# Kernel optimization log

Hardware: AMD Instinct MI355X
Metric: run time of the kernel (lower is better)

## Reference

```python
import jax, jax.numpy as jnp
from jax import lax
import numpy as np

K_TOP = 100
NMS_THRESH = 0.5
SUBJECT_CATEGORY_ID = 0


def box_cxcywh_to_xyxy(b):
    cx, cy, w, h = b[..., 0], b[..., 1], b[..., 2], b[..., 3]
    return jnp.stack([cx - 0.5 * w, cy - 0.5 * h, cx + 0.5 * w, cy + 0.5 * h], axis=-1)


def _pairwise_iou(boxes):
    # boxes: [K,4] xyxy; uses the +1 pixel convention from the original numpy NMS
    x1, y1, x2, y2 = boxes[:, 0], boxes[:, 1], boxes[:, 2], boxes[:, 3]
    area = (x2 - x1 + 1.0) * (y2 - y1 + 1.0)
    xx1 = jnp.maximum(x1[:, None], x1[None, :])
    yy1 = jnp.maximum(y1[:, None], y1[None, :])
    xx2 = jnp.minimum(x2[:, None], x2[None, :])
    yy2 = jnp.minimum(y2[:, None], y2[None, :])
    w = jnp.maximum(0.0, xx2 - xx1 + 1.0)
    h = jnp.maximum(0.0, yy2 - yy1 + 1.0)
    inter = w * h
    union = area[:, None] + area[None, :] - inter
    return inter / union


def _nms_keep(sub_boxes, obj_boxes, obj_labels, hoi_scores):
    # Greedy grouped pairwise NMS for one image.
    # Grouping key degenerates to object label (subject cat and verb-row are constant).
    K = sub_boxes.shape[0]
    max_scores = hoi_scores.max(axis=-1)
    order = jnp.argsort(-max_scores)
    ovr = _pairwise_iou(sub_boxes) * _pairwise_iou(obj_boxes)  # [K,K]
    same_group = obj_labels[:, None] == obj_labels[None, :]
    ovr = jnp.where(same_group, ovr, 0.0)
    ovr_s = ovr[order][:, order]
    upper = jnp.triu(jnp.ones((K, K), dtype=bool), k=1)
    sup_mat = (ovr_s > NMS_THRESH) & upper  # suppression only of later (lower-score) items

    def body(i, st):
        suppressed, keep = st
        ki = jnp.logical_not(suppressed[i])
        keep = keep.at[i].set(ki)
        suppressed = suppressed | (ki & sup_mat[i])
        return suppressed, keep

    _, keep_sorted = lax.fori_loop(0, K, body, (jnp.zeros(K, bool), jnp.zeros(K, bool)))
    return jnp.zeros(K, bool).at[order].set(keep_sorted)


def setup_inputs() -> dict:
    key = jax.random.key(0)
    k1, k2, k3, k4, k5, k6 = jax.random.split(key, 6)
    B, Q, C, V = 256, 300, 81, 117
    return {
        "pred_obj_logits": jax.random.normal(k1, (B, Q, C), dtype=jnp.float32),
        "pred_verb_logits": jax.random.normal(k2, (B, Q, V), dtype=jnp.float32),
        "pred_sub_boxes": jax.random.uniform(k3, (B, Q, 4), dtype=jnp.float32),
        "pred_obj_boxes": jax.random.uniform(k4, (B, Q, 4), dtype=jnp.float32),
        "correct_mat": (jax.random.uniform(k5, (V, C), dtype=jnp.float32) > 0.3).astype(jnp.float32),
        "target_sizes": jax.random.randint(k6, (B, 2), 200, 640, dtype=jnp.int32),
    }


def reference(pred_obj_logits, pred_verb_logits, pred_sub_boxes, pred_obj_boxes, correct_mat, target_sizes):
    B, Q, C = pred_obj_logits.shape
    V = pred_verb_logits.shape[-1]

    obj_prob = jax.nn.softmax(pred_obj_logits, axis=-1)       # [B,Q,C]  (no_obj=False)
    verb_scores = jax.nn.sigmoid(pred_verb_logits)            # [B,Q,V]

    topk_values, topk_indexes = lax.top_k(obj_prob.reshape(B, Q * C), K_TOP)  # [B,100]
    topk_boxes = topk_indexes // C
    obj_labels = topk_indexes % C

    vs = jnp.take_along_axis(verb_scores, topk_boxes[..., None], axis=1)      # [B,100,V]
    ob = jnp.take_along_axis(pred_obj_boxes, topk_boxes[..., None], axis=1)   # [B,100,4]
    sb = jnp.take_along_axis(pred_sub_boxes, topk_boxes[..., None], axis=1)

    img_h = target_sizes[:, 0].astype(jnp.float32)
    img_w = target_sizes[:, 1].astype(jnp.float32)
    scale_fct = jnp.stack([img_w, img_h, img_w, img_h], axis=1)  # [B,4]
    sub_boxes = box_cxcywh_to_xyxy(sb) * scale_fct[:, None, :]
    obj_boxes = box_cxcywh_to_xyxy(ob) * scale_fct[:, None, :]

    hoi_scores = vs * topk_values[..., None]                    # [B,100,V]
    # masks[b,k,v] = correct_mat[v, obj_labels[b,k]]
    masks = correct_mat.T[obj_labels]                           # [B,100,V]
    hoi_scores = hoi_scores * masks

    keep = jax.vmap(_nms_keep)(sub_boxes, obj_boxes, obj_labels, hoi_scores)  # [B,100] bool
    final_scores = hoi_scores * keep[..., None].astype(hoi_scores.dtype)

    return final_scores, topk_values, obj_labels, sub_boxes, obj_boxes, keep
```

## Files before the change

### kernel.cpp

```cpp
#include <hip/hip_runtime.h>
#include <cmath>

#pragma clang fp contract(off)

#define NT 1024
constexpr int B_ = 256, Q_ = 300, C_ = 81, V_ = 117, K_ = 100;
constexpr int QC_ = Q_ * C_;
constexpr int KV_ = K_ * V_;
constexpr int CAP = 1024;
constexpr int CMN = V_ * C_;

using u32 = unsigned int;
using u64 = unsigned long long;
using u16 = unsigned short;
using u8  = unsigned char;

constexpr u32 PCUT_BITS = 0x3C000000u;
constexpr int BIN0 = 480;
constexpr int NB   = 64;
constexpr int HREP = 8;

constexpr int OFF_CM   = 0;
constexpr int OFF_HIST = 37920;
constexpr int OFF_RMAX = OFF_HIST + 8192;
constexpr int OFF_RINV = OFF_RMAX + 1240;
constexpr int OFF_BSUB = OFF_RINV + 1240;
constexpr int OFF_BOBJ = OFF_BSUB + 1600;
constexpr int OFF_SUPR = OFF_BOBJ + 1600;
constexpr int OFF_SELV = OFF_SUPR + 1600;
constexpr int OFF_SELI = OFF_SELV + 400;
constexpr int OFF_MAXB = OFF_SELI + 400;
constexpr int OFF_ORD  = OFF_MAXB + 400;
constexpr int OFF_LAB  = OFF_ORD + 104;
constexpr int OFF_MISC = OFF_LAB + 104;
constexpr int SMEM_SZ  = OFF_MISC + 48;
static_assert(SMEM_SZ <= 65536, "LDS overflow");
static_assert((OFF_BSUB & 15) == 0 && (OFF_BOBJ & 15) == 0, "b128 align");
static_assert(OFF_HIST >= OFF_CM + CMN * 4, "cm/hist overlap");
static_assert((OFF_HIST & 15) == 0, "cand/hist align");

__device__ __forceinline__ void bar_lds() {
    asm volatile("s_waitcnt lgkmcnt(0)\n\ts_barrier" ::: "memory");
}

__device__ __forceinline__ int RM(int r) { return r + (r >> 5); }

__device__ __forceinline__ u64 shfl_xor_u64(u64 v, int mask) {
    u32 lo = (u32)v, hi = (u32)(v >> 32);
    lo = (u32)__shfl_xor((int)lo, mask, 64);
    hi = (u32)__shfl_xor((int)hi, mask, 64);
    return ((u64)hi << 32) | lo;
}

template <int CTRL>
__device__ __forceinline__ int dpp_i(int x) {
    return __builtin_amdgcn_update_dpp(0, x, CTRL, 0xF, 0xF, true);
}
__device__ __forceinline__ float bfly16(float x){ return __int_as_float(__builtin_amdgcn_ds_swizzle(__float_as_int(x), 0x401F)); }
__device__ __forceinline__ float bfly8 (float x){ return __int_as_float(dpp_i<0x128>(__float_as_int(x))); }
__device__ __forceinline__ float bfly4 (float x){ return __int_as_float(__builtin_amdgcn_ds_swizzle(__float_as_int(x), 0x101F)); }
__device__ __forceinline__ float bfly2 (float x){ return __int_as_float(dpp_i<0x4E>(__float_as_int(x))); }
__device__ __forceinline__ float bfly1 (float x){ return __int_as_float(dpp_i<0xB1>(__float_as_int(x))); }
__device__ __forceinline__ int ibfly4(int x){ return __builtin_amdgcn_ds_swizzle(x, 0x101F); }
__device__ __forceinline__ int ibfly2(int x){ return dpp_i<0x4E>(x); }
__device__ __forceinline__ int ibfly1(int x){ return dpp_i<0xB1>(x); }

__device__ __forceinline__ float iou4(float4 a, float4 b, float areaSum) {
    float xx1 = fmaxf(a.x, b.x);
    float yy1 = fmaxf(a.y, b.y);
    float xx2 = fminf(a.z, b.z);
    float yy2 = fminf(a.w, b.w);
    float w = fmaxf(0.f, xx2 - xx1 + 1.f);
    float h = fmaxf(0.f, yy2 - yy1 + 1.f);
    float inter = w * h;
    return inter / (areaSum - inter);
}

__global__ __launch_bounds__(NT, 4) void hoi_kernel(
    const float* __restrict__ obj_logits,
    const float* __restrict__ verb_logits,
    const float* __restrict__ sub_boxes_in,
    const float* __restrict__ obj_boxes_in,
    const float* __restrict__ cm,
    const int*   __restrict__ tsizes,
    float* __restrict__ out)
{
    const int b = blockIdx.x;
    const int tid = threadIdx.x;

    __shared__ __align__(16) u8 smem[SMEM_SZ];
    float* cml     = (float*)(smem + OFF_CM);
    u32*   hist    = (u32*)(smem + OFF_HIST);
    u64*   cand    = (u64*)(smem + OFF_HIST);
    float* asub    = (float*)(smem + OFF_HIST);
    float* aobj    = (float*)(smem + OFF_HIST + 512);
    float* rowmax  = (float*)(smem + OFF_RMAX);
    float* rinv    = (float*)(smem + OFF_RINV);
    float (*bsub)[4]   = (float(*)[4])(smem + OFF_BSUB);
    float (*bobj)[4]   = (float(*)[4])(smem + OFF_BOBJ);
    u32   (*supcol)[4] = (u32(*)[4])(smem + OFF_SUPR);
    float* sel_val = (float*)(smem + OFF_SELV);
    u32*   sel_idx = (u32*)(smem + OFF_SELI);
    u32*   maxbits = (u32*)(smem + OFF_MAXB);
    u8*    order8  = (u8*)(smem + OFF_ORD);
    u8*    lab8    = (u8*)(smem + OFF_LAB);
    u32*   skeep     = (u32*)(smem + OFF_MISC);
    u32*   keep_bits = (u32*)(smem + OFF_MISC + 16);
    u32*   s_cnt     = (u32*)(smem + OFF_MISC + 32);
    int*   sT        = (int*)(smem + OFF_MISC + 36);
    u64*   wred    = (u64*)(smem + OFF_BOBJ);
    u64*   s_prev  = (u64*)(smem + OFF_SUPR);

    const float* lg = obj_logits + (size_t)b * QC_;

    float* o0 = out;
    float* o1 = out + (size_t)B_ * KV_;
    float* o2 = o1 + (size_t)B_ * K_;
    float* o3 = o2 + (size_t)B_ * K_;
    float* o4 = o3 + (size_t)B_ * K_ * 4;
    float* o5 = o4 + (size_t)B_ * K_ * 4;

    if (tid < NB * HREP) hist[tid] = 0;
    if (tid == 0) *s_cnt = 0;
    bar_lds();

    const int g = tid >> 5, l = tid & 31;
    const bool have2 = (l < C_ - 64);
    const int hsub = tid & (HREP - 1);
    u32 cmask = 0;
    {
        float v0[10], v1[10], v2[10];
        #pragma unroll
        for (int s = 0; s < 10; ++s) {
            int r = g + 32 * s;
            const float* row = lg + (size_t)((r < Q_ ? r : Q_ - 1) * C_);
            v0[s] = row[l];
            v1[s] = row[l + 32];
            v2[s] = have2 ? row[l + 64] : -INFINITY;
        }
        float m[10];
        #pragma unroll
        for (int s = 0; s < 10; ++s) m[s] = fmaxf(fmaxf(v0[s], v1[s]), v2[s]);
        #pragma unroll
        for (int s = 0; s < 10; ++s) m[s] = fmaxf(m[s], bfly16(m[s]));
        #pragma unroll
        for (int s = 0; s < 10; ++s) m[s] = fmaxf(m[s], bfly8(m[s]));
        #pragma unroll
        for (int s = 0; s < 10; ++s) m[s] = fmaxf(m[s], bfly4(m[s]));
        #pragma unroll
        for (int s = 0; s < 10; ++s) m[s] = fmaxf(m[s], bfly2(m[s]));
        #pragma unroll
        for (int s = 0; s < 10; ++s) m[s] = fmaxf(m[s], bfly1(m[s]));
        float e0[10], e1[10], e2[10], sm[10];
        #pragma unroll
        for (int s = 0; s < 10; ++s) {
            e0[s] = expf(v0[s] - m[s]);
            e1[s] = expf(v1[s] - m[s]);
            e2[s] = have2 ? expf(v2[s] - m[s]) : 0.f;
            sm[s] = e0[s] + e1[s] + e2[s];
        }
        #pragma unroll
        for (int s = 0; s < 10; ++s) sm[s] += bfly16(sm[s]);
        #pragma unroll
        for (int s = 0; s < 10; ++s) sm[s] += bfly8(sm[s]);
        #pragma unroll
        for (int s = 0; s < 10; ++s) sm[s] += bfly4(sm[s]);
        #pragma unroll
        for (int s = 0; s < 10; ++s) sm[s] += bfly2(sm[s]);
        #pragma unroll
        for (int s = 0; s < 10; ++s) sm[s] += bfly1(sm[s]);
        #pragma unroll
        for (int s = 0; s < 10; ++s) {
            int r = g + 32 * s;
            if (r < Q_) {
                float ri = 1.f / sm[s];
                float p0 = e0[s] * ri, p1 = e1[s] * ri;
                u32 x0 = __float_as_uint(p0), x1 = __float_as_uint(p1);
                if (x0 >= PCUT_BITS) {
                    atomicAdd(&hist[(((x0 >> 21) - BIN0) << 3) + hsub], 1u);
                    cmask |= 1u << (3 * s);
                }
                if (x1 >= PCUT_BITS) {
                    atomicAdd(&hist[(((x1 >> 21) - BIN0) << 3) + hsub], 1u);
                    cmask |= 1u << (3 * s + 1);
                }
                if (have2) {
                    float p2 = e2[s] * ri;
                    u32 x2 = __float_as_uint(p2);
                    if (x2 >= PCUT_BITS) {
                        atomicAdd(&hist[(((x2 >> 21) - BIN0) << 3) + hsub], 1u);
                        cmask |= 1u << (3 * s + 2);
                    }
                }
                if (l == 0) { rowmax[RM(r)] = m[s]; rinv[RM(r)] = ri; }
            }
        }
    }
    bar_lds();

    if (tid < 64) {
        uint4 ha = ((const uint4*)hist)[tid * 2];
        uint4 hb = ((const uint4*)hist)[tid * 2 + 1];
        u32 suf = ha.x + ha.y + ha.z + ha.w + hb.x + hb.y + hb.z + hb.w;
        #pragma unroll
        for (int off = 1; off < 64; off <<= 1) {
            u32 o = (u32)__shfl_down((int)suf, off, 64);
            suf += (tid + off < 64) ? o : 0;
        }
        u32 nxt = (u32)__shfl_down((int)suf, 1, 64);
        if (tid == 63) nxt = 0;
        if (suf >= (u32)K_ && nxt < (u32)K_) *sT = BIN0 + tid;
    }
    bar_lds();
    const int T = *sT;

    u32 mk = cmask;
    while (mk) {
        int bpos = (int)__builtin_ctz(mk);
        mk &= mk - 1;
        int s = (bpos * 171) >> 9;
        int c = bpos - 3 * s;
        int r = g + 32 * s;
        int col = l + 32 * c;
        int i = r * C_ + col;
        float p = expf(lg[i] - rowmax[RM(r)]) * rinv[RM(r)];
        u32 xb = __float_as_uint(p);
        if ((int)(xb >> 21) >= T) {
            u32 pos = atomicAdd(s_cnt, 1u);
            if (pos < (u32)CAP)
                cand[pos] = ((u64)xb << 32) | (u32)(~i);
        }
    }
    bar_lds();
    const int ncand = (int)*s_cnt;

    constexpr int CM4 = CMN / 4;
    const float4* cmg4 = (const float4*)cm;
    float4 cc0 = cmg4[tid];
    float4 cc1 = cmg4[tid + NT];
    float4 cc2 = (tid < CM4 - 2 * NT) ? cmg4[tid + 2 * NT]
                                      : make_float4(0.f, 0.f, 0.f, 0.f);
    float ctail = (tid == 0) ? cm[CMN - 1] : 0.f;

    if (ncand <= CAP) {
        if (tid < ncand) {
            u64 mykey = cand[tid];
            int rank = 0;
            int f = 0;
            for (; f + 4 <= ncand; f += 4) {
                u64 k0 = cand[f], k1 = cand[f + 1];
                u64 k2 = cand[f + 2], k3 = cand[f + 3];
                rank += (k0 > mykey) ? 1 : 0;
                rank += (k1 > mykey) ? 1 : 0;
                rank += (k2 > mykey) ? 1 : 0;
                rank += (k3 > mykey) ? 1 : 0;
            }
            for (; f < ncand; ++f) rank += (cand[f] > mykey) ? 1 : 0;
            if (rank < K_) {
                sel_val[rank] = __uint_as_float((u32)(mykey >> 32));
                sel_idx[rank] = ~(u32)mykey;
            }
        }
    } else {
        if (tid == 0) *s_prev = ~0ull;
        __syncthreads();
        for (int r = 0; r < K_; r++) {
            u64 prev = *s_prev;
            u64 local = 0;
            for (int i = tid; i < QC_; i += NT) {
                int q = i / C_;
                float p = expf(lg[i] - rowmax[RM(q)]) * rinv[RM(q)];
                u64 key = ((u64)__float_as_uint(p) << 32) | (u32)(~i);
                if (key < prev && key > local) local = key;
            }
            for (int off = 32; off > 0; off >>= 1) {
                u64 o = shfl_xor_u64(local, off);
                if (o > local) local = o;
            }
            if ((tid & 63) == 0) wred[tid >> 6] = local;
            __syncthreads();
            if (tid == 0) {
                u64 m = wred[0];
                for (int wv = 1; wv < 16; wv++) if (wred[wv] > m) m = wred[wv];
                *s_prev = m;
                u32 idx = ~(u32)m;
                if (idx >= (u32)QC_) idx = 0;
                sel_val[r] = __uint_as_float((u32)(m >> 32));
                sel_idx[r] = idx;
            }
            __syncthreads();
        }
    }

    ((float4*)cml)[tid] = cc0;
    ((float4*)cml)[tid + NT] = cc1;
    if (tid < CM4 - 2 * NT) ((float4*)cml)[tid + 2 * NT] = cc2;
    if (tid == 0) cml[CMN - 1] = ctail;
    bar_lds();

    if (tid < 800) {
        int c = tid >> 3, j = tid & 7;
        u32 idx = sel_idx[c];
        int q = (int)idx / C_, lab = (int)idx - q * C_;
        const float* vrow = verb_logits + ((size_t)b * Q_ + q) * V_;
        float* orow = o0 + (size_t)b * KV_ + c * V_;
        float sv = sel_val[c];
        float m = 0.f;
        #pragma unroll
        for (int k = 0; k < 15; ++k) {
            int v = j + 8 * k;
            if (v < V_) {
                float x = vrow[v];
                float cv = cml[v * C_ + lab];
                float hv = (1.f / (1.f + expf(-x))) * sv * cv;
                orow[v] = hv;
                m = fmaxf(m, hv);
            }
        }
        m = fmaxf(m, bfly4(m));
        m = fmaxf(m, bfly2(m));
        m = fmaxf(m, bfly1(m));
        if (j == 0) { maxbits[c] = __float_as_uint(m); lab8[c] = (u8)lab; }
    } else if (tid < 900) {
        int t = tid - 800;
        int idx = (int)sel_idx[t];
        int q = idx / C_;
        float iw = (float)tsizes[b * 2 + 1];
        float ih = (float)tsizes[b * 2 + 0];
        float4 sb = ((const float4*)sub_boxes_in)[(size_t)b * Q_ + q];
        float x1 = (sb.x - 0.5f * sb.z) * iw, y1 = (sb.y - 0.5f * sb.w) * ih;
        float x2 = (sb.x + 0.5f * sb.z) * iw, y2 = (sb.y + 0.5f * sb.w) * ih;
        bsub[t][0] = x1; bsub[t][1] = y1; bsub[t][2] = x2; bsub[t][3] = y2;
        asub[t] = (x2 - x1 + 1.f) * (y2 - y1 + 1.f);
        supcol[t][0] = 0; supcol[t][1] = 0; supcol[t][2] = 0; supcol[t][3] = 0;
    } else if (tid < 1000) {
        int t = tid - 900;
        int idx = (int)sel_idx[t];
        int q = idx / C_;
        float iw = (float)tsizes[b * 2 + 1];
        float ih = (float)tsizes[b * 2 + 0];
        float4 ob = ((const float4*)obj_boxes_in)[(size_t)b * Q_ + q];
        float x1 = (ob.x - 0.5f * ob.z) * iw, y1 = (ob.y - 0.5f * ob.w) * ih;
        float x2 = (ob.x + 0.5f * ob.z) * iw, y2 = (ob.y + 0.5f * ob.w) * ih;
        bobj[t][0] = x1; bobj[t][1] = y1; bobj[t][2] = x2; bobj[t][3] = y2;
        aobj[t] = (x2 - x1 + 1.f) * (y2 - y1 + 1.f);
    } else if (tid < 1004) {
        keep_bits[tid - 1000] = 0;
    }
    bar_lds();

    if (tid < 800) {
        int r = tid >> 3, j = tid & 7;
        u64 kr = ((u64)maxbits[r] << 32) | (u32)(~r);
        int rank = 0;
        for (int k = 0; k < 13; k++) {
            int jj = j * 13 + k;
            if (jj < K_) {
                u64 kj = ((u64)maxbits[jj] << 32) | (u32)(~jj);
                rank += (kj > kr) ? 1 : 0;
            }
        }
        rank += ibfly4(rank);
        rank += ibfly2(rank);
        rank += ibfly1(rank);
        if (j == 0) order8[rank] = (u8)r;
    }
    bar_lds();

    if (tid < K_) {
        o1[(size_t)b * K_ + tid] = sel_val[tid];
        o2[(size_t)b * K_ + tid] = (float)(sel_idx[tid] % (u32)C_);
    }
    if (tid >= 128 && tid < 128 + K_ * 4) {
        int t = tid - 128;
        int r = t >> 2, k = t & 3;
        o3[((size_t)b * K_) * 4 + t] = bsub[r][k];
        o4[((size_t)b * K_) * 4 + t] = bobj[r][k];
    }

    for (int e = tid; e < K_ * K_; e += NT) {
        int i = e / K_, j = e - i * K_;
        if (j > i) {
            int ri = order8[i], rj = order8[j];
            u32 li = lab8[ri], lj = lab8[rj];
            if (li == lj) {
                float4 s_i = *(const float4*)bsub[ri];
                float4 s_j = *(const float4*)bsub[rj];
                float4 b_i = *(const float4*)bobj[ri];
                float4 b_j = *(const float4*)bobj[rj];
                float o = iou4(s_i, s_j, asub[ri] + asub[rj]) *
                          iou4(b_i, b_j, aobj[ri] + aobj[rj]);
                if (o > 0.5f)
                    atomicOr(&supcol[j][i >> 5], 1u << (i & 31));
            }
        }
    }
    bar_lds();

    if (tid < 64) {
        u32 cA[4], cB[4];
        #pragma unroll
        for (int w = 0; w < 4; ++w) cA[w] = supcol[tid][w];
        #pragma unroll
        for (int w = 0; w < 4; ++w) cB[w] = (tid < K_ - 64) ? supcol[tid + 64][w] : 0u;
        bool sA = false, sB = false;
        u32 km[4] = {0, 0, 0, 0};
        #pragma unroll
        for (int i = 0; i < 64; ++i) {
            u64 bal = __ballot(sA);
            if (!((bal >> i) & 1)) {
                km[i >> 5] |= 1u << (i & 31);
                sA = sA || ((cA[i >> 5] >> (i & 31)) & 1u);
                sB = sB || ((cB[i >> 5] >> (i & 31)) & 1u);
            }
        }
        #pragma unroll
        for (int i = 64; i < K_; ++i) {
            u64 bal = __ballot(sB);
            if (!((bal >> (i - 64)) & 1)) {
                km[i >> 5] |= 1u << (i & 31);
                sA = sA || ((cA[i >> 5] >> (i & 31)) & 1u);
                sB = sB || ((cB[i >> 5] >> (i & 31)) & 1u);
            }
        }
        if (tid == 0) { skeep[0] = km[0]; skeep[1] = km[1]; skeep[2] = km[2]; skeep[3] = km[3]; }
    }
    bar_lds();
    if (tid < K_) {
        if ((skeep[tid >> 5] >> (tid & 31)) & 1u) {
            int r = order8[tid];
            atomicOr(&keep_bits[r >> 5], 1u << (r & 31));
        }
    }
    __syncthreads();

    for (int f = tid; f < KV_; f += NT) {
        int r = f / V_;
        if (!((keep_bits[r >> 5] >> (r & 31)) & 1u))
            o0[(size_t)b * KV_ + f] = 0.f;
    }
    if (tid < K_) {
        bool kp = (keep_bits[tid >> 5] >> (tid & 31)) & 1u;
        o5[(size_t)b * K_ + tid] = kp ? 1.f : 0.f;
    }
}

extern "C" void kernel_launch(void* const* d_in, const int* in_sizes, int n_in,
                              void* d_out, int out_size, void* d_ws, size_t ws_size,
                              hipStream_t stream) {
    const float* obj_logits  = (const float*)d_in[0];
    const float* verb_logits = (const float*)d_in[1];
    const float* sub_boxes   = (const float*)d_in[2];
    const float* obj_boxes   = (const float*)d_in[3];
    const float* cm          = (const float*)d_in[4];
    const int*   ts          = (const int*)d_in[5];
    hipLaunchKernelGGL(hoi_kernel, dim3(B_), dim3(NT), 0, stream,
                       obj_logits, verb_logits, sub_boxes, obj_boxes, cm, ts,
                       (float*)d_out);
}
```

Baseline: 127.8 us.

## Map one wavefront per top-k row for verb scoring with prefetched next row

The verb-score stage now gives each of the 16 wavefronts a strided set of top-k rows, one lane per verb. Each wavefront prefetches the next row's logits while computing the current one, instead of using 8 threads per row over 800 threads. Box loads are issued before that loop and converted after it, so their latency overlaps. The final zeroing of suppressed rows also goes row-per-wavefront, which drops the per-element division. The cost is serial iteration per wavefront (about 7 rows) and more registers.

```diff
diff --git a/kernel.cpp b/kernel.cpp
--- a/kernel.cpp
+++ b/kernel.cpp
@@ -298,54 +298,85 @@
     if (tid == 0) cml[CMN - 1] = ctail;
     bar_lds();
 
-    if (tid < 800) {
-        int c = tid >> 3, j = tid & 7;
+    const int w = tid >> 6, lane = tid & 63;
+    const int off0 = lane * C_;
+    const int off1 = (lane + 64) * C_;
+    const bool l53 = (lane < V_ - 64);
+
+    const bool doSub = (tid < K_);
+    const bool doObj = (tid >= 512 && tid < 512 + K_);
+    float4 boxv = make_float4(0.f, 0.f, 0.f, 0.f);
+    float biw = 0.f, bih = 0.f;
+    if (doSub || doObj) {
+        int t = doSub ? tid : tid - 512;
+        int idx = (int)sel_idx[t];
+        int q = idx / C_;
+        biw = (float)tsizes[b * 2 + 1];
+        bih = (float)tsizes[b * 2 + 0];
+        boxv = doSub ? ((const float4*)sub_boxes_in)[(size_t)b * Q_ + q]
+                     : ((const float4*)obj_boxes_in)[(size_t)b * Q_ + q];
+    }
+    if (tid >= 200 && tid < 200 + K_) {
+        int t = tid - 200;
+        supcol[t][0] = 0; supcol[t][1] = 0; supcol[t][2] = 0; supcol[t][3] = 0;
+    } else if (tid >= 320 && tid < 324) {
+        keep_bits[tid - 320] = 0;
+    }
+
+    {
+        const float* vbase = verb_logits + (size_t)b * Q_ * V_;
+        float* obase = o0 + (size_t)b * KV_;
+        int c = w;
         u32 idx = sel_idx[c];
         int q = (int)idx / C_, lab = (int)idx - q * C_;
-        const float* vrow = verb_logits + ((size_t)b * Q_ + q) * V_;
-        float* orow = o0 + (size_t)b * KV_ + c * V_;
         float sv = sel_val[c];
-        float m = 0.f;
-        #pragma unroll
-        for (int k = 0; k < 15; ++k) {
-            int v = j + 8 * k;
-            if (v < V_) {
-                float x = vrow[v];
-                float cv = cml[v * C_ + lab];
-                float hv = (1.f / (1.f + expf(-x))) * sv * cv;
-                orow[v] = hv;
-                m = fmaxf(m, hv);
-            }
-        }
-        m = fmaxf(m, bfly4(m));
-        m = fmaxf(m, bfly2(m));
-        m = fmaxf(m, bfly1(m));
-        if (j == 0) { maxbits[c] = __float_as_uint(m); lab8[c] = (u8)lab; }
-    } else if (tid < 900) {
-        int t = tid - 800;
-        int idx = (int)sel_idx[t];
-        int q = idx / C_;
-        float iw = (float)tsizes[b * 2 + 1];
-        float ih = (float)tsizes[b * 2 + 0];
-        float4 sb = ((const float4*)sub_boxes_in)[(size_t)b * Q_ + q];
-        float x1 = (sb.x - 0.5f * sb.z) * iw, y1 = (sb.y - 0.5f * sb.w) * ih;
-        float x2 = (sb.x + 0.5f * sb.z) * iw, y2 = (sb.y + 0.5f * sb.w) * ih;
-        bsub[t][0] = x1; bsub[t][1] = y1; bsub[t][2] = x2; bsub[t][3] = y2;
-        asub[t] = (x2 - x1 + 1.f) * (y2 - y1 + 1.f);
-        supcol[t][0] = 0; supcol[t][1] = 0; supcol[t][2] = 0; supcol[t][3] = 0;
-    } else if (tid < 1000) {
-        int t = tid - 900;
-        int idx = (int)sel_idx[t];
-        int q = idx / C_;
-        float iw = (float)tsizes[b * 2 + 1];
-        float ih = (float)tsizes[b * 2 + 0];
-        float4 ob = ((const float4*)obj_boxes_in)[(size_t)b * Q_ + q];
-        float x1 = (ob.x - 0.5f * ob.z) * iw, y1 = (ob.y - 0.5f * ob.w) * ih;
-        float x2 = (ob.x + 0.5f * ob.z) * iw, y2 = (ob.y + 0.5f * ob.w) * ih;
-        bobj[t][0] = x1; bobj[t][1] = y1; bobj[t][2] = x2; bobj[t][3] = y2;
-        aobj[t] = (x2 - x1 + 1.f) * (y2 - y1 + 1.f);
-    } else if (tid < 1004) {
-        keep_bits[tid - 1000] = 0;
+        const float* vr = vbase + (size_t)q * V_;
+        float x0 = vr[lane];
+        float x1 = l53 ? vr[lane + 64] : 0.f;
+        while (true) {
+            int cn = c + 16;
+            int labn = 0; float svn = 0.f, x0n = 0.f, x1n = 0.f;
+            if (cn < K_) {
+                u32 idxn = sel_idx[cn];
+                int qn = (int)idxn / C_;
+                labn = (int)idxn - qn * C_;
+                svn = sel_val[cn];
+                const float* vrn = vbase + (size_t)qn * V_;
+                x0n = vrn[lane];
+                x1n = l53 ? vrn[lane + 64] : 0.f;
+            }
+            float cv0 = cml[off0 + lab];
+            float cv1 = l53 ? cml[off1 + lab] : 0.f;
+            float h0 = (1.f / (1.f + expf(-x0))) * sv * cv0;
+            float h1 = l53 ? (1.f / (1.f + expf(-x1))) * sv * cv1 : 0.f;
+            float* orow = obase + c * V_;
+            orow[lane] = h0;
+            if (l53) orow[lane + 64] = h1;
+            float m = fmaxf(h0, h1);
+            m = fmaxf(m, __shfl_xor(m, 32, 64));
+            m = fmaxf(m, bfly16(m));
+            m = fmaxf(m, bfly8(m));
+            m = fmaxf(m, bfly4(m));
+            m = fmaxf(m, bfly2(m));
+            m = fmaxf(m, bfly1(m));
+            if (lane == 0) { maxbits[c] = __float_as_uint(m); lab8[c] = (u8)lab; }
+            if (cn >= K_) break;
+            c = cn; lab = labn; sv = svn; x0 = x0n; x1 = x1n;
+        }
+    }
+
+    if (doSub) {
+        int t = tid;
+        float x1v = (boxv.x - 0.5f * boxv.z) * biw, y1v = (boxv.y - 0.5f * boxv.w) * bih;
+        float x2v = (boxv.x + 0.5f * boxv.z) * biw, y2v = (boxv.y + 0.5f * boxv.w) * bih;
+        bsub[t][0] = x1v; bsub[t][1] = y1v; bsub[t][2] = x2v; bsub[t][3] = y2v;
+        asub[t] = (x2v - x1v + 1.f) * (y2v - y1v + 1.f);
+    } else if (doObj) {
+        int t = tid - 512;
+        float x1v = (boxv.x - 0.5f * boxv.z) * biw, y1v = (boxv.y - 0.5f * boxv.w) * bih;
+        float x2v = (boxv.x + 0.5f * boxv.z) * biw, y2v = (boxv.y + 0.5f * boxv.w) * bih;
+        bobj[t][0] = x1v; bobj[t][1] = y1v; bobj[t][2] = x2v; bobj[t][3] = y2v;
+        aobj[t] = (x2v - x1v + 1.f) * (y2v - y1v + 1.f);
     }
     bar_lds();
 
@@ -400,9 +431,9 @@
     if (tid < 64) {
         u32 cA[4], cB[4];
         #pragma unroll
-        for (int w = 0; w < 4; ++w) cA[w] = supcol[tid][w];
-        #pragma unroll
-        for (int w = 0; w < 4; ++w) cB[w] = (tid < K_ - 64) ? supcol[tid + 64][w] : 0u;
+        for (int ww = 0; ww < 4; ++ww) cA[ww] = supcol[tid][ww];
+        #pragma unroll
+        for (int ww = 0; ww < 4; ++ww) cB[ww] = (tid < K_ - 64) ? supcol[tid + 64][ww] : 0u;
         bool sA = false, sB = false;
         u32 km[4] = {0, 0, 0, 0};
         #pragma unroll
@@ -434,10 +465,12 @@
     }
     __syncthreads();
 
-    for (int f = tid; f < KV_; f += NT) {
-        int r = f / V_;
-        if (!((keep_bits[r >> 5] >> (r & 31)) & 1u))
-            o0[(size_t)b * KV_ + f] = 0.f;
+    for (int c = w; c < K_; c += 16) {
+        if (!((keep_bits[c >> 5] >> (c & 31)) & 1u)) {
+            float* orow = o0 + (size_t)b * KV_ + c * V_;
+            orow[lane] = 0.f;
+            if (l53) orow[lane + 64] = 0.f;
+        }
     }
     if (tid < K_) {
         bool kp = (keep_bits[tid >> 5] >> (tid & 31)) & 1u;
```

New measurement: 128.5 us. No clear change (+0.5%).
